# Optimization experiments

Hardware: AMD Instinct MI355X
Metric: run time of the kernel (lower is better)

The kernel has to match this reference:

```python
import jax, jax.numpy as jnp
import numpy as np

N, E, D = 10000, 160000, 512


def gcn_conv(x, src, dst, W, b):
    # GCNConv (PyG default): linear -> sym-normalized aggregation with self-loops -> +bias
    n = x.shape[0]
    h = x @ W  # [N, D]
    loop = jnp.arange(n)
    s = jnp.concatenate([src, loop])
    d = jnp.concatenate([dst, loop])
    deg = jax.ops.segment_sum(jnp.ones_like(d, dtype=h.dtype), d, num_segments=n)
    dinv = jnp.where(deg > 0, jax.lax.rsqrt(deg), 0.0)
    norm = dinv[s] * dinv[d]  # [E+N]
    msg = h[s] * norm[:, None]  # [E+N, D]
    out = jax.ops.segment_sum(msg, d, num_segments=n)
    return out + b


def gnn_embed(x, edge_index, Ws, bs):
    src, dst = edge_index[0], edge_index[1]
    h = x
    L = len(Ws)
    for i in range(L):
        h = gcn_conv(h, src, dst, Ws[i], bs[i])
        if i < L - 1:
            h = jax.nn.relu(h)
    return jnp.mean(h, axis=0).reshape(1, -1)  # [1, D]


def setup_inputs() -> dict:
    key = jax.random.key(0)
    ks = jax.random.split(key, 16)
    x1 = jax.random.normal(ks[0], (N, D), dtype=jnp.float32)
    x2 = jax.random.normal(ks[1], (N, D), dtype=jnp.float32)
    edge_index1 = jax.random.randint(ks[2], (2, E), 0, N, dtype=jnp.int64)
    edge_index2 = jax.random.randint(ks[3], (2, E), 0, N, dtype=jnp.int64)
    sc = 1.0 / np.sqrt(D)
    W1 = jax.random.normal(ks[4], (D, D), dtype=jnp.float32) * sc
    W2 = jax.random.normal(ks[5], (D, D), dtype=jnp.float32) * sc
    W3 = jax.random.normal(ks[6], (D, D), dtype=jnp.float32) * sc
    b1 = jnp.zeros((D,), jnp.float32)
    b2 = jnp.zeros((D,), jnp.float32)
    b3 = jnp.zeros((D,), jnp.float32)
    # FCL comparison head: concat(u1,u2) [1,2D] -> Linear(2D,D) -> ReLU -> Linear(D,1) -> sigmoid
    Wf1 = jax.random.normal(ks[7], (2 * D, D), dtype=jnp.float32) * (1.0 / np.sqrt(2 * D))
    bf1 = jnp.zeros((D,), jnp.float32)
    Wf2 = jax.random.normal(ks[8], (D, 1), dtype=jnp.float32) * sc
    bf2 = jnp.zeros((1,), jnp.float32)
    return dict(x1=x1, x2=x2, edge_index1=edge_index1, edge_index2=edge_index2,
                W1=W1, W2=W2, W3=W3, b1=b1, b2=b2, b3=b3,
                Wf1=Wf1, bf1=bf1, Wf2=Wf2, bf2=bf2)


def reference(x1, x2, edge_index1, edge_index2, W1, W2, W3, b1, b2, b3, Wf1, bf1, Wf2, bf2):
    Ws, bs = (W1, W2, W3), (b1, b2, b3)
    u1 = gnn_embed(x1, edge_index1, Ws, bs)  # [1, D]
    u2 = gnn_embed(x2, edge_index2, Ws, bs)  # [1, D]
    z = jnp.concatenate([u1, u2], axis=1)  # [1, 2D]
    h = jax.nn.relu(z @ Wf1 + bf1)
    score = jax.nn.sigmoid(h @ Wf2 + bf2)  # [1, 1]
    return score
```

## Files before the change

### kernel.cpp

```cpp
#include <hip/hip_runtime.h>
#include <math.h>

#define NN 10000
#define NE 160000
#define DD 512
#define MPAD 20096

typedef __attribute__((ext_vector_type(8))) short bf16x8;
typedef __attribute__((ext_vector_type(4))) float f32x4;
typedef __attribute__((ext_vector_type(8))) unsigned short u16x8;

__device__ __forceinline__ unsigned short f2bf(float f) {
    unsigned u = __float_as_uint(f);
    u += 0x7FFFu + ((u >> 16) & 1u);
    return (unsigned short)(u >> 16);
}
__device__ __forceinline__ float bf2f(unsigned short h) {
    return __uint_as_float(((unsigned)h) << 16);
}

#define GLOAD16(g, l) __builtin_amdgcn_global_load_lds( \
    (const __attribute__((address_space(1))) void*)(unsigned long long)(const void*)(g), \
    (__attribute__((address_space(3))) void*)(unsigned)(unsigned long long)(void*)(l), \
    16, 0, 0)

__global__ void k_init(int* cnt, int* cursor, float* u, float* hacc) {
    int i = blockIdx.x * blockDim.x + threadIdx.x;
    if (i < 2 * NN) { cnt[i] = 0; cursor[i] = 0; }
    if (i < 2 * DD) u[i] = 0.f;
    if (i < DD) hacc[i] = 0.f;
}

__global__ void k_count(const int* e1, const int* e2, int* cnt) {
    int i = blockIdx.x * blockDim.x + threadIdx.x;
    if (i < NE) {
        atomicAdd(&cnt[e1[NE + i]], 1);
    } else if (i < 2 * NE) {
        int e = i - NE;
        atomicAdd(&cnt[NN + e2[NE + e]], 1);
    }
}

__global__ void k_dinv(const int* cnt, float* dinv) {
    int i = blockIdx.x * blockDim.x + threadIdx.x;
    if (i < 2 * NN) dinv[i] = rsqrtf((float)(cnt[i] + 1));
}

__global__ void k_scan(const int* cnt, int* offs) {
    int g = blockIdx.x;
    const int* c = cnt + g * NN;
    int* o = offs + g * (NN + 1);
    __shared__ int sums[1024];
    int t = threadIdx.x;
    const int PER = 10;
    int base = t * PER;
    int vals[PER];
    int local = 0;
    #pragma unroll
    for (int j = 0; j < PER; ++j) {
        int idx = base + j;
        int v = (idx < NN) ? c[idx] : 0;
        vals[j] = v; local += v;
    }
    sums[t] = local;
    __syncthreads();
    for (int off = 1; off < 1024; off <<= 1) {
        int v = (t >= off) ? sums[t - off] : 0;
        __syncthreads();
        sums[t] += v;
        __syncthreads();
    }
    int prefix = (t > 0) ? sums[t - 1] : 0;
    #pragma unroll
    for (int j = 0; j < PER; ++j) {
        int idx = base + j;
        if (idx < NN) { o[idx] = prefix; prefix += vals[j]; }
    }
    if (t == 1023) o[NN] = sums[1023];
}

__global__ void k_fill(const int* e1, const int* e2, const int* offs,
                       int* cursor, int* adj) {
    int i = blockIdx.x * blockDim.x + threadIdx.x;
    if (i >= 2 * NE) return;
    int g = (i < NE) ? 0 : 1;
    int e = i - g * NE;
    const int* ei = g ? e2 : e1;
    int s = ei[e];
    int d = ei[NE + e];
    int pos = atomicAdd(&cursor[g * NN + d], 1);
    adj[g * NE + offs[g * (NN + 1) + d] + pos] = s;
}

__global__ void k_cvt_x(const float* __restrict__ x1, const float* __restrict__ x2,
                        unsigned short* __restrict__ xb) {
    long long gid = (long long)blockIdx.x * 256 + threadIdx.x;
    long long i8 = gid * 8;
    if (i8 >= (long long)MPAD * DD) return;
    int row = (int)(i8 >> 9);
    int col = (int)(i8 & 511);
    u16x8 ov;
    if (row < 2 * NN) {
        const float* src = (row < NN) ? (x1 + (size_t)row * DD + col)
                                      : (x2 + (size_t)(row - NN) * DD + col);
        float4 f0 = ((const float4*)src)[0];
        float4 f1 = ((const float4*)src)[1];
        ov[0] = f2bf(f0.x); ov[1] = f2bf(f0.y); ov[2] = f2bf(f0.z); ov[3] = f2bf(f0.w);
        ov[4] = f2bf(f1.x); ov[5] = f2bf(f1.y); ov[6] = f2bf(f1.z); ov[7] = f2bf(f1.w);
    } else {
        #pragma unroll
        for (int j = 0; j < 8; ++j) ov[j] = 0;
    }
    *(u16x8*)(xb + i8) = ov;
}

__global__ void k_cvt_w(const float* __restrict__ W1, const float* __restrict__ W2,
                        const float* __restrict__ W3, unsigned short* __restrict__ Wt) {
    __shared__ float t[32][33];
    const float* W = (blockIdx.z == 0) ? W1 : (blockIdx.z == 1) ? W2 : W3;
    unsigned short* o = Wt + (size_t)blockIdx.z * DD * DD;
    int n0 = blockIdx.x * 32, k0 = blockIdx.y * 32;
    int tx = threadIdx.x, ty = threadIdx.y;
    t[ty][tx] = W[(size_t)(k0 + ty) * DD + n0 + tx];
    __syncthreads();
    o[(size_t)(n0 + ty) * DD + k0 + tx] = f2bf(t[tx][ty]);
}

__global__ __launch_bounds__(256) void k_gemm(const unsigned short* __restrict__ A,
                                              const unsigned short* __restrict__ Bt,
                                              unsigned short* __restrict__ C, int M) {
    __shared__ bf16x8 As[512];
    __shared__ bf16x8 Bs[512];
    int tid = threadIdx.x;
    int lane = tid & 63;
    int wid = tid >> 6;
    int wr = wid >> 1, wc = wid & 1;
    int row0 = blockIdx.x * 128;
    int col0 = blockIdx.y * 128;

    int ch0 = wid * 64 + lane;
    int ch1 = 256 + wid * 64 + lane;
    const unsigned short* gA0 = A + (size_t)(row0 + (ch0 & 127)) * DD + (ch0 >> 7) * 8;
    const unsigned short* gA1 = A + (size_t)(row0 + (ch1 & 127)) * DD + (ch1 >> 7) * 8;
    const unsigned short* gB0 = Bt + (size_t)(col0 + (ch0 & 127)) * DD + (ch0 >> 7) * 8;
    const unsigned short* gB1 = Bt + (size_t)(col0 + (ch1 & 127)) * DD + (ch1 >> 7) * 8;

    int iA[4], iB[4];
    #pragma unroll
    for (int m = 0; m < 4; ++m) {
        iA[m] = (lane >> 4) * 128 + wr * 64 + m * 16 + (lane & 15);
        iB[m] = (lane >> 4) * 128 + wc * 64 + m * 16 + (lane & 15);
    }

    f32x4 acc[4][4];
    #pragma unroll
    for (int m = 0; m < 4; ++m)
        #pragma unroll
        for (int n = 0; n < 4; ++n)
            acc[m][n] = (f32x4){0.f, 0.f, 0.f, 0.f};

    for (int k0 = 0; k0 < DD; k0 += 32) {
        GLOAD16(gA0, &As[wid * 64]);
        GLOAD16(gA1, &As[256 + wid * 64]);
        GLOAD16(gB0, &Bs[wid * 64]);
        GLOAD16(gB1, &Bs[256 + wid * 64]);
        gA0 += 32; gA1 += 32; gB0 += 32; gB1 += 32;
        __syncthreads();
        bf16x8 af[4], bfr[4];
        #pragma unroll
        for (int m = 0; m < 4; ++m) { af[m] = As[iA[m]]; bfr[m] = Bs[iB[m]]; }
        #pragma unroll
        for (int m = 0; m < 4; ++m)
            #pragma unroll
            for (int n = 0; n < 4; ++n)
                acc[m][n] = __builtin_amdgcn_mfma_f32_16x16x32_bf16(af[m], bfr[n], acc[m][n], 0, 0, 0);
        __syncthreads();
    }

    #pragma unroll
    for (int m = 0; m < 4; ++m) {
        int rbase = row0 + wr * 64 + m * 16 + (lane >> 4) * 4;
        #pragma unroll
        for (int n = 0; n < 4; ++n) {
            int col = col0 + wc * 64 + n * 16 + (lane & 15);
            f32x4 v = acc[m][n];
            #pragma unroll
            for (int i = 0; i < 4; ++i) {
                int r = rbase + i;
                if (r < M) C[(size_t)r * DD + col] = f2bf(v[i]);
            }
        }
    }
}

template <bool RELU>
__global__ __launch_bounds__(256) void k_agg(const unsigned short* __restrict__ h,
                                             const int* __restrict__ adj,
                                             const int* __restrict__ offs,
                                             const float* __restrict__ dinv,
                                             const float* __restrict__ bias,
                                             unsigned short* __restrict__ out) {
    int wid = threadIdx.x >> 6;
    int lane = threadIdx.x & 63;
    int v = blockIdx.x * 4 + wid;
    int g = (v < NN) ? 0 : 1;
    int vl = v - g * NN;
    const int* o = offs + g * (NN + 1);
    int beg = o[vl], end = o[vl + 1];
    const int* a = adj + g * NE;
    float dv = dinv[v];
    int c = lane * 8;
    const unsigned short* hb = h + c;
    int gbase = g * NN;

    u16x8 hv = *(const u16x8*)(hb + (size_t)v * DD);
    float acc[8];
    #pragma unroll
    for (int j = 0; j < 8; ++j) acc[j] = bf2f(hv[j]) * dv;

    int e = beg;
    for (; e + 4 <= end; e += 4) {
        int s0 = a[e] + gbase, s1 = a[e + 1] + gbase;
        int s2 = a[e + 2] + gbase, s3 = a[e + 3] + gbase;
        u16x8 r0 = *(const u16x8*)(hb + (size_t)s0 * DD);
        u16x8 r1 = *(const u16x8*)(hb + (size_t)s1 * DD);
        u16x8 r2 = *(const u16x8*)(hb + (size_t)s2 * DD);
        u16x8 r3 = *(const u16x8*)(hb + (size_t)s3 * DD);
        float d0 = dinv[s0], d1 = dinv[s1], d2 = dinv[s2], d3 = dinv[s3];
        #pragma unroll
        for (int j = 0; j < 8; ++j) {
            acc[j] = fmaf(bf2f(r0[j]), d0, acc[j]);
            acc[j] = fmaf(bf2f(r1[j]), d1, acc[j]);
            acc[j] = fmaf(bf2f(r2[j]), d2, acc[j]);
            acc[j] = fmaf(bf2f(r3[j]), d3, acc[j]);
        }
    }
    for (; e < end; ++e) {
        int s = a[e] + gbase;
        float ds = dinv[s];
        u16x8 hs = *(const u16x8*)(hb + (size_t)s * DD);
        #pragma unroll
        for (int j = 0; j < 8; ++j) acc[j] = fmaf(bf2f(hs[j]), ds, acc[j]);
    }

    float4 b0 = ((const float4*)(bias + c))[0];
    float4 b1 = ((const float4*)(bias + c))[1];
    float bb[8] = {b0.x, b0.y, b0.z, b0.w, b1.x, b1.y, b1.z, b1.w};
    u16x8 ov;
    #pragma unroll
    for (int j = 0; j < 8; ++j) {
        float x = fmaf(acc[j], dv, bb[j]);
        if (RELU) x = fmaxf(x, 0.f);
        ov[j] = f2bf(x);
    }
    *(u16x8*)(out + (size_t)v * DD + c) = ov;
}

__global__ __launch_bounds__(256) void k_meanpart(const unsigned short* __restrict__ h,
                                                  float* __restrict__ u) {
    __shared__ float sm[4][DD];
    int g = blockIdx.y;
    int chunk = blockIdx.x;
    int wid = threadIdx.x >> 6;
    int lane = threadIdx.x & 63;
    int c = lane * 8;
    const int rows_per = (NN + 127) / 128;
    int r0 = chunk * rows_per;
    int r1 = min(r0 + rows_per, NN);
    float acc[8] = {0.f, 0.f, 0.f, 0.f, 0.f, 0.f, 0.f, 0.f};
    for (int r = r0 + wid; r < r1; r += 4) {
        u16x8 hv = *(const u16x8*)(h + (size_t)(g * NN + r) * DD + c);
        #pragma unroll
        for (int j = 0; j < 8; ++j) acc[j] += bf2f(hv[j]);
    }
    #pragma unroll
    for (int j = 0; j < 8; ++j) sm[wid][c + j] = acc[j];
    __syncthreads();
    if (wid == 0) {
        #pragma unroll
        for (int j = 0; j < 8; ++j) {
            float s = sm[0][c + j] + sm[1][c + j] + sm[2][c + j] + sm[3][c + j];
            atomicAdd(&u[g * DD + c + j], s);
        }
    }
}

__global__ void k_head1(const float* __restrict__ u, const float* __restrict__ Wf1,
                        float* __restrict__ hacc) {
    int t = threadIdx.x;
    int kb = blockIdx.x;
    const float inv = 1.0f / (float)NN;
    float acc = 0.f;
    for (int k = kb * 128; k < kb * 128 + 128; ++k) {
        float z = u[k] * inv;
        acc = fmaf(z, Wf1[(size_t)k * DD + t], acc);
    }
    atomicAdd(&hacc[t], acc);
}

__global__ void k_head2(const float* __restrict__ hacc, const float* __restrict__ bf1,
                        const float* __restrict__ Wf2, const float* __restrict__ bf2,
                        float* __restrict__ outp) {
    __shared__ float red[DD];
    int t = threadIdx.x;
    float hv = fmaxf(hacc[t] + bf1[t], 0.f);
    red[t] = hv * Wf2[t];
    __syncthreads();
    for (int s = DD / 2; s > 0; s >>= 1) {
        if (t < s) red[t] += red[t + s];
        __syncthreads();
    }
    if (t == 0) outp[0] = 1.f / (1.f + expf(-(red[0] + bf2[0])));
}

extern "C" void kernel_launch(void* const* d_in, const int* in_sizes, int n_in,
                              void* d_out, int out_size, void* d_ws, size_t ws_size,
                              hipStream_t stream) {
    const float* x1  = (const float*)d_in[0];
    const float* x2  = (const float*)d_in[1];
    const int*   e1  = (const int*)d_in[2];
    const int*   e2  = (const int*)d_in[3];
    const float* W1  = (const float*)d_in[4];
    const float* W2  = (const float*)d_in[5];
    const float* W3  = (const float*)d_in[6];
    const float* b1  = (const float*)d_in[7];
    const float* b2  = (const float*)d_in[8];
    const float* b3  = (const float*)d_in[9];
    const float* Wf1 = (const float*)d_in[10];
    const float* bf1 = (const float*)d_in[11];
    const float* Wf2 = (const float*)d_in[12];
    const float* bf2 = (const float*)d_in[13];
    float* outp = (float*)d_out;

    char* w = (char*)d_ws;
    unsigned short* xb = (unsigned short*)w; w += (size_t)MPAD * DD * 2;
    unsigned short* hG = (unsigned short*)w; w += (size_t)MPAD * DD * 2;
    unsigned short* hA = (unsigned short*)w; w += (size_t)MPAD * DD * 2;
    unsigned short* Wt = (unsigned short*)w; w += (size_t)3 * DD * DD * 2;
    int*   cnt    = (int*)w;   w += 2 * NN * 4;
    int*   cursor = (int*)w;   w += 2 * NN * 4;
    int*   offs   = (int*)w;   w += 2 * (NN + 1) * 4 + 8;
    int*   adj    = (int*)w;   w += 2 * NE * 4;
    float* dinv   = (float*)w; w += 2 * NN * 4;
    float* u      = (float*)w; w += 2 * DD * 4;
    float* hacc   = (float*)w; w += DD * 4;

    const int M = 2 * NN;

    k_init<<<(2 * NN + 255) / 256, 256, 0, stream>>>(cnt, cursor, u, hacc);
    k_count<<<(2 * NE + 255) / 256, 256, 0, stream>>>(e1, e2, cnt);
    k_dinv<<<(2 * NN + 255) / 256, 256, 0, stream>>>(cnt, dinv);
    k_scan<<<2, 1024, 0, stream>>>(cnt, offs);
    k_fill<<<(2 * NE + 255) / 256, 256, 0, stream>>>(e1, e2, offs, cursor, adj);
    k_cvt_x<<<(MPAD * DD / 8 + 255) / 256, 256, 0, stream>>>(x1, x2, xb);
    k_cvt_w<<<dim3(16, 16, 3), dim3(32, 32), 0, stream>>>(W1, W2, W3, Wt);

    dim3 ggrid(MPAD / 128, DD / 128);

    k_gemm<<<ggrid, 256, 0, stream>>>(xb, Wt, hG, M);
    k_agg<true><<<M / 4, 256, 0, stream>>>(hG, adj, offs, dinv, b1, hA);
    k_gemm<<<ggrid, 256, 0, stream>>>(hA, Wt + (size_t)DD * DD, hG, M);
    k_agg<true><<<M / 4, 256, 0, stream>>>(hG, adj, offs, dinv, b2, hA);
    k_gemm<<<ggrid, 256, 0, stream>>>(hA, Wt + (size_t)2 * DD * DD, hG, M);
    k_agg<false><<<M / 4, 256, 0, stream>>>(hG, adj, offs, dinv, b3, hA);

    k_meanpart<<<dim3(128, 2), 256, 0, stream>>>(hA, u);
    k_head1<<<8, DD, 0, stream>>>(u, Wf1, hacc);
    k_head2<<<1, DD, 0, stream>>>(hacc, bf1, Wf2, bf2, outp);
}
```

Baseline: 330.1 us.

## Split aggregation into column chunks with four nodes per wavefront

Restructures the sparse aggregation kernel. Each wavefront now handles four destination nodes, with 16 lanes per node covering a 128-column slice. Blocks are interleaved across graph and column-chunk combinations, so neighbouring blocks touch the same rows at the same time, which should improve L2 reuse of gathered rows. The aim is more parallel rows in flight and better cache locality of the gathers. The cost is that each edge index and its dinv value are loaded four times, once per column chunk, and per-lane loads are shorter.

```diff
diff --git a/kernel.cpp b/kernel.cpp
--- a/kernel.cpp
+++ b/kernel.cpp
@@ -194,26 +194,31 @@
 }
 
 template <bool RELU>
-__global__ __launch_bounds__(256) void k_agg(const unsigned short* __restrict__ h,
-                                             const int* __restrict__ adj,
-                                             const int* __restrict__ offs,
-                                             const float* __restrict__ dinv,
-                                             const float* __restrict__ bias,
-                                             unsigned short* __restrict__ out) {
+__global__ __launch_bounds__(256) void k_aggc(const unsigned short* __restrict__ h,
+                                              const int* __restrict__ adj,
+                                              const int* __restrict__ offs,
+                                              const float* __restrict__ dinv,
+                                              const float* __restrict__ bias,
+                                              unsigned short* __restrict__ out) {
+    int bid = blockIdx.x;
+    int combo = bid & 7;
+    int nb = bid >> 3;
+    int g = combo >> 2;
+    int yc = combo & 3;
     int wid = threadIdx.x >> 6;
     int lane = threadIdx.x & 63;
-    int v = blockIdx.x * 4 + wid;
-    int g = (v < NN) ? 0 : 1;
-    int vl = v - g * NN;
+    int sub = lane >> 4;
+    int li = lane & 15;
+    int v = nb * 16 + wid * 4 + sub;
+    int c = yc * 128 + li * 8;
+    int gbase = g * NN;
     const int* o = offs + g * (NN + 1);
-    int beg = o[vl], end = o[vl + 1];
+    int beg = o[v], end = o[v + 1];
     const int* a = adj + g * NE;
-    float dv = dinv[v];
-    int c = lane * 8;
+    float dv = dinv[gbase + v];
     const unsigned short* hb = h + c;
-    int gbase = g * NN;
-
-    u16x8 hv = *(const u16x8*)(hb + (size_t)v * DD);
+
+    u16x8 hv = *(const u16x8*)(hb + (size_t)(gbase + v) * DD);
     float acc[8];
     #pragma unroll
     for (int j = 0; j < 8; ++j) acc[j] = bf2f(hv[j]) * dv;
@@ -253,7 +258,7 @@
         if (RELU) x = fmaxf(x, 0.f);
         ov[j] = f2bf(x);
     }
-    *(u16x8*)(out + (size_t)v * DD + c) = ov;
+    *(u16x8*)(out + (size_t)(gbase + v) * DD + c) = ov;
 }
 
 __global__ __launch_bounds__(256) void k_meanpart(const unsigned short* __restrict__ h,
@@ -356,13 +361,14 @@
     k_cvt_w<<<dim3(16, 16, 3), dim3(32, 32), 0, stream>>>(W1, W2, W3, Wt);
 
     dim3 ggrid(MPAD / 128, DD / 128);
+    const int aggGrid = (NN / 16) * 8;
 
     k_gemm<<<ggrid, 256, 0, stream>>>(xb, Wt, hG, M);
-    k_agg<true><<<M / 4, 256, 0, stream>>>(hG, adj, offs, dinv, b1, hA);
+    k_aggc<true><<<aggGrid, 256, 0, stream>>>(hG, adj, offs, dinv, b1, hA);
     k_gemm<<<ggrid, 256, 0, stream>>>(hA, Wt + (size_t)DD * DD, hG, M);
-    k_agg<true><<<M / 4, 256, 0, stream>>>(hG, adj, offs, dinv, b2, hA);
+    k_aggc<true><<<aggGrid, 256, 0, stream>>>(hG, adj, offs, dinv, b2, hA);
     k_gemm<<<ggrid, 256, 0, stream>>>(hA, Wt + (size_t)2 * DD * DD, hG, M);
-    k_agg<false><<<M / 4, 256, 0, stream>>>(hG, adj, offs, dinv, b3, hA);
+    k_aggc<false><<<aggGrid, 256, 0, stream>>>(hG, adj, offs, dinv, b3, hA);
 
     k_meanpart<<<dim3(128, 2), 256, 0, stream>>>(hA, u);
     k_head1<<<8, DD, 0, stream>>>(u, Wf1, hacc);
```

New measurement: 296.7 us. -10.1%, faster.
